# Optimization experiments

Measured on AMD Instinct MI355X. Metric: run time of the kernel, lower is better.

## Reference

```python
import jax, jax.numpy as jnp
import numpy as np
from jax import lax

MAX_DEPTH = 8
NLEAVES = 2 ** MAX_DEPTH      # 256
NNODES = 2 ** MAX_DEPTH - 1   # 255 (preorder-numbered inner nodes)
NCLASS = 10
EPS = 1e-5
BATCH = 8192


def _build_paths():
    # Reproduce the torch preorder node numbering and DFS leaf numbering.
    node_ctr = [0]
    leaf_paths = []
    def rec(depth, path):
        idx = node_ctr[0]; node_ctr[0] += 1
        if depth < MAX_DEPTH:
            rec(depth + 1, path + [(idx, 0)])   # left child: prob (1 - p)
            rec(depth + 1, path + [(idx, 1)])   # right child: prob p
        else:
            leaf_paths.append(path + [(idx, 0)])
            leaf_paths.append(path + [(idx, 1)])
    rec(1, [])
    nidx = np.array([[n for n, _ in p] for p in leaf_paths], dtype=np.int32)  # [L, D]
    dirs = np.array([[d for _, d in p] for p in leaf_paths], dtype=bool)      # [L, D]
    return nidx, dirs

NODE_IDX, DIRS = _build_paths()


def _bn(x, g, b):
    # training-mode batchnorm over all dims except channel axis 1 (biased var)
    axes = tuple(i for i in range(x.ndim) if i != 1)
    m = x.mean(axes, keepdims=True)
    v = x.var(axes, keepdims=True)
    shape = [1] * x.ndim; shape[1] = -1
    return (x - m) * lax.rsqrt(v + EPS) * g.reshape(shape) + b.reshape(shape)


def _conv(x, w, b):
    y = lax.conv_general_dilated(x, w, (1, 1), 'VALID',
                                 dimension_numbers=('NCHW', 'OIHW', 'NCHW'))
    return y + b[None, :, None, None]


def _pool2(x):
    return lax.reduce_window(x, -jnp.inf, lax.max, (1, 1, 2, 2), (1, 1, 2, 2), 'VALID')


def setup_inputs() -> dict:
    ks = jax.random.split(jax.random.key(0), 12)
    f32 = jnp.float32
    return {
        'x': jax.random.normal(ks[0], (BATCH, 1, 28, 28), f32),
        'y': jax.random.randint(ks[1], (BATCH,), 0, NCLASS),
        'conv1_w': 0.1 * jax.random.normal(ks[2], (20, 1, 5, 5), f32),
        'conv1_b': jnp.zeros((20,), f32),
        'conv2_w': 0.05 * jax.random.normal(ks[3], (50, 20, 5, 5), f32),
        'conv2_b': jnp.zeros((50,), f32),
        'g1': jnp.ones((20,), f32), 'be1': jnp.zeros((20,), f32),
        'g2': jnp.ones((50,), f32), 'be2': jnp.zeros((50,), f32),
        'fc1_w': 0.05 * jax.random.normal(ks[4], (10, 800), f32),
        'fc1_b': jnp.zeros((10,), f32),
        'g3': jnp.ones((10,), f32), 'be3': jnp.zeros((10,), f32),
        'theta_w': 0.3 * jax.random.normal(ks[5], (NNODES, 10), f32),
        'theta_b': jnp.zeros((NNODES,), f32),
        'pi': jax.random.uniform(ks[6], (NLEAVES, NCLASS), f32, 0.1, 1.0),
    }


def reference(x, y, conv1_w, conv1_b, conv2_w, conv2_b, g1, be1, g2, be2,
              fc1_w, fc1_b, g3, be3, theta_w, theta_b, pi):
    B = x.shape[0]
    # CNN backbone
    h = _pool2(jax.nn.relu(_bn(_conv(x, conv1_w, conv1_b), g1, be1)))
    h = _pool2(jax.nn.relu(_bn(_conv(h, conv2_w, conv2_b), g2, be2)))
    h = h.reshape(B, 4 * 4 * 50)
    h = jax.nn.relu(_bn(h @ fc1_w.T + fc1_b, g3, be3))        # [B, 10]
    # batched soft-tree gating: one fused GEMM for all 255 tiny Linear(10,1)
    p = jax.nn.sigmoid(h @ theta_w.T + theta_b)                # [B, NNODES]
    g = p[:, NODE_IDX]                                         # [B, L, D]
    mu = jnp.prod(jnp.where(DIRS[None], g, 1.0 - g), axis=2)   # [B, L]
    # pi is a row-stochastic distribution (uniform at torch init)
    pi_n = pi / pi.sum(1, keepdims=True)
    # stale P from __init__: uniform mu (1/L) @ pi  ->  column means of pi
    P_prev = jnp.broadcast_to(pi_n.mean(0), (B, NCLASS))       # [B, C]
    # vectorized cal_pi (soft-EM update of leaf distributions)
    Y = jax.nn.one_hot(y, NCLASS, dtype=mu.dtype)              # [B, C]
    S = mu.T @ (Y / P_prev)                                    # [L, C]
    pi_h = pi_n * S
    pi_new = pi_h / pi_h.sum(1, keepdims=True)
    # cal_P and log
    P = mu @ pi_new                                            # [B, C]
    return jnp.log(P)
```

## Files before the change

### kernel.cpp

```cpp
#include <hip/hip_runtime.h>
#include <hip/hip_bf16.h>
#include <math.h>

typedef __attribute__((ext_vector_type(8))) short short8v;
typedef __attribute__((ext_vector_type(4))) float float4v;

static const size_t F_RAWP1B = 0;
static const size_t F_C2P    = 14155776;
static const size_t F_PART1  = 20709376;
static const size_t F_PART2  = 21037056;
static const size_t F_PART3  = 21241856;
static const size_t F_BN1    = 21246976;
static const size_t F_BN2    = 21247016;
static const size_t F_SRAW   = 21247136;
static const size_t F_WB2    = 21252256;
static const size_t F_WB1    = 21271712;
static const size_t F_SPART  = 21272224;
static const size_t F_HRAW   = 0;
static const size_t F_MU     = 81920;

__device__ __forceinline__ float relu_(float v) { return v > 0.f ? v : 0.f; }

__device__ __forceinline__ unsigned int pack_bf16x2(float a, float b) {
  __hip_bfloat16 ha = __float2bfloat16(a), hb = __float2bfloat16(b);
  unsigned short ua, ub;
  __builtin_memcpy(&ua, &ha, 2); __builtin_memcpy(&ub, &hb, 2);
  return ((unsigned int)ub << 16) | ua;
}

__device__ __forceinline__ unsigned short cvt_bf16(float a) {
  __hip_bfloat16 h = __float2bfloat16(a);
  unsigned short u; __builtin_memcpy(&u, &h, 2);
  return u;
}

__device__ __forceinline__ float pick_(float a, float b, bool mx) {
  return mx ? fmaxf(a, b) : fminf(a, b);
}

__global__ __launch_bounds__(256) void k_wprep(
    const float* __restrict__ w1, const float* __restrict__ w2,
    unsigned short* __restrict__ wb1, unsigned short* __restrict__ wb2)
{
  const int gi = blockIdx.x * 256 + threadIdx.x;
  if (gi < 1024) {
    const int n = gi >> 5, k = gi & 31;
    const int kh = k / 6, kw = k - kh*6;
    float v = (n < 20 && kh < 5 && kw < 5) ? w1[n*25 + kh*5 + kw] : 0.f;
    wb1[gi] = cvt_bf16(v);
  } else {
    const int idx = gi - 1024;
    const int cc = idx >> 9;
    const int rem = idx & 511;
    const int n = rem >> 3, j = rem & 7;
    float v = 0.f;
    if (cc < 75 && n < 50) {
      const int khw = cc / 3, icg = cc - khw*3;
      const int ic = icg*8 + j;
      if (ic < 20) {
        const int kh = khw / 5, kw = khw - kh*5;
        v = w2[((n*20 + ic)*5 + kh)*5 + kw];
      }
    }
    wb2[idx] = cvt_bf16(v);
  }
}

__global__ __launch_bounds__(256) void k_conv1_mfma(
    const float* __restrict__ x, const unsigned short* __restrict__ wb1,
    const float* __restrict__ g1, unsigned int* __restrict__ rawp1b,
    float* __restrict__ part)
{
  __shared__ alignas(16) unsigned short xpk[2][1568];
  __shared__ float sred[4][32], qred[4][32];
  const int tid = threadIdx.x, blk = blockIdx.x;
  const int img0 = blk * 4;
  const int wave = tid >> 6, lane = tid & 63, lo = lane & 15, hi = lane >> 4;

  const short8v bfr0 = *(const short8v*)(wb1 + (lo*32 + hi*8));
  const short8v bfr1 = *(const short8v*)(wb1 + ((16+lo)*32 + hi*8));
  const unsigned enc = (hi==0) ? 0x0E020100u
                     : (hi==1) ? 0x1D1C100Fu
                     : (hi==2) ? 0x2C2B2A1Eu
                     :           0x003A3938u;
  const int off0 = enc & 255, off1 = (enc>>8)&255, off2 = (enc>>16)&255, off3 = enc>>24;
  const int pb   = (lo & 1) * 392;
  const int oyp  = (lo >> 1) & 1, qoff = lo >> 2;
  const int inv  = pb + (6*wave + oyp)*14;
  const bool gp0 = (g1[lo] >= 0.f);
  const bool gp1 = (lo < 4) ? (g1[16+lo] >= 0.f) : true;
  const int sr = tid >> 3, sq = tid & 7;
  const bool act = (tid < 224) && (sq < 7);
  const int su0 = sr*7 + sq;
  const int su1 = 196 + su0;

  float4 sv = make_float4(0.f, 0.f, 0.f, 0.f);
  if (act) sv = *(const float4*)(x + (size_t)img0 * 784 + sr*28 + 4*sq);
  {
    float n0 = __shfl_down(sv.x, 1);
    n0 = (sq == 6) ? 0.f : n0;
    if (act) {
      uint2* xb2 = (uint2*)&xpk[0][0];
      uint2 t0; t0.x = pack_bf16x2(sv.x, sv.y); t0.y = pack_bf16x2(sv.z, sv.w);
      uint2 t1; t1.x = pack_bf16x2(sv.y, sv.z); t1.y = pack_bf16x2(sv.w, n0);
      xb2[su0] = t0;
      xb2[su1] = t1;
    }
  }
  __syncthreads();

  float bs0[3] = {0.f, 0.f, 0.f}, bq0[3] = {0.f, 0.f, 0.f};
  float bs1[3] = {0.f, 0.f, 0.f}, bq1[3] = {0.f, 0.f, 0.f};
  int cur = 0;
  for (int ii = 0; ii < 4; ++ii) {
    if (ii < 3 && act)
      sv = *(const float4*)(x + (size_t)(img0 + ii + 1) * 784 + sr*28 + 4*sq);
    const unsigned int* xpd = (const unsigned int*)&xpk[cur][0];
    unsigned int* dst = rawp1b + (size_t)(img0 + ii) * 1728;

    #pragma unroll 1
    for (int g = 0; g < 3; ++g) {
      float4v acc[3][2];
      #pragma unroll
      for (int t3 = 0; t3 < 3; ++t3) {
        acc[t3][0] = (float4v){0.f,0.f,0.f,0.f};
        acc[t3][1] = (float4v){0.f,0.f,0.f,0.f};
      }
      #pragma unroll
      for (int t3 = 0; t3 < 3; ++t3) {
        const int base = inv + g*28 + t3*4 + qoff;
        union { unsigned int u[4]; short8v v; } cu;
        cu.u[0] = xpd[base + off0];
        cu.u[1] = xpd[base + off1];
        cu.u[2] = xpd[base + off2];
        cu.u[3] = xpd[base + off3];
        acc[t3][0] = __builtin_amdgcn_mfma_f32_16x16x32_bf16(cu.v, bfr0, acc[t3][0], 0, 0, 0);
        acc[t3][1] = __builtin_amdgcn_mfma_f32_16x16x32_bf16(cu.v, bfr1, acc[t3][1], 0, 0, 0);
      }
      #pragma unroll
      for (int t3 = 0; t3 < 3; ++t3) {
        const int T = wave*9 + g*3 + t3;
        const int q = T*4 + hi;
        const float4v v0 = acc[t3][0];
        const float4v v1 = acc[t3][1];
        #pragma unroll
        for (int r = 0; r < 4; ++r) { bs0[t3] += v0[r]; bq0[t3] += v0[r]*v0[r]; }
        #pragma unroll
        for (int r = 0; r < 4; ++r) { bs1[t3] += v1[r]; bq1[t3] += v1[r]*v1[r]; }
        const float p0 = pick_(pick_(v0[0], v0[1], gp0), pick_(v0[2], v0[3], gp0), gp0);
        const float p1 = pick_(pick_(v1[0], v1[1], gp1), pick_(v1[2], v1[3], gp1), gp1);
        const float o0 = __shfl_down(p0, 1);
        const float o1 = __shfl_down(p1, 1);
        if ((lo & 1) == 0) {
          dst[q*12 + (lo >> 1)] = pack_bf16x2(p0, o0);
          if (lo < 8)
            dst[q*12 + 8 + (lo >> 1)] = pack_bf16x2(p1, o1);
        }
      }
    }

    if (ii < 3) {
      float n0 = __shfl_down(sv.x, 1);
      n0 = (sq == 6) ? 0.f : n0;
      if (act) {
        uint2* xb2 = (uint2*)&xpk[cur ^ 1][0];
        uint2 t0; t0.x = pack_bf16x2(sv.x, sv.y); t0.y = pack_bf16x2(sv.z, sv.w);
        uint2 t1; t1.x = pack_bf16x2(sv.y, sv.z); t1.y = pack_bf16x2(sv.w, n0);
        xb2[su0] = t0;
        xb2[su1] = t1;
      }
    }
    __syncthreads();
    cur ^= 1;
  }

  float bsv0 = bs0[0] + bs0[1] + bs0[2], bqv0 = bq0[0] + bq0[1] + bq0[2];
  float bsv1 = bs1[0] + bs1[1] + bs1[2], bqv1 = bq1[0] + bq1[1] + bq1[2];
  bsv0 += __shfl_down(bsv0, 32); bqv0 += __shfl_down(bqv0, 32);
  bsv0 += __shfl_down(bsv0, 16); bqv0 += __shfl_down(bqv0, 16);
  bsv1 += __shfl_down(bsv1, 32); bqv1 += __shfl_down(bqv1, 32);
  bsv1 += __shfl_down(bsv1, 16); bqv1 += __shfl_down(bqv1, 16);
  if (hi == 0) {
    sred[wave][lo] = bsv0; sred[wave][16+lo] = bsv1;
    qred[wave][lo] = bqv0; qred[wave][16+lo] = bqv1;
  }
  __syncthreads();
  if (tid < 20) {
    float s = 0.f, q = 0.f;
    #pragma unroll
    for (int w2 = 0; w2 < 4; ++w2) { s += sred[w2][tid]; q += qred[w2][tid]; }
    part[(size_t)blk*40 + tid]      = s;
    part[(size_t)blk*40 + 20 + tid] = q;
  }
}

__global__ __launch_bounds__(256) void k_conv2_mfma(
    const unsigned int* __restrict__ rawp1b, const unsigned short* __restrict__ wb,
    const float* __restrict__ bn1, const float* __restrict__ g2,
    float* __restrict__ c2p, float* __restrict__ part)
{
  __shared__ alignas(16) unsigned int in4[6912];
  __shared__ float sred[4][64], qred[4][64];
  __shared__ alignas(16) float bn1i[48];
  __shared__ unsigned short aofft[76];
  const int tid = threadIdx.x, blk = blockIdx.x;
  if (tid < 24) {
    const float sc = (tid < 20) ? bn1[tid]      : 0.f;
    const float sh = (tid < 20) ? bn1[20 + tid] : 0.f;
    bn1i[2*tid] = sc; bn1i[2*tid + 1] = sh;
  }
  if (tid < 76) {
    const int cc2 = tid > 74 ? 74 : tid;
    const int khw = cc2 / 3, icg = cc2 - khw*3;
    const int kh = khw / 5, kw = khw - kh*5;
    aofft[tid] = (unsigned short)((kh*12 + kw)*48 + icg*16);
  }
  __syncthreads();

  const uint4* src4 = (const uint4*)(rawp1b + (size_t)blk * 6912);
  uint4* dst4 = (uint4*)in4;
  int jj = tid % 3;
  for (int k = 0; k < 7; ++k) {
    const int i = k*256 + tid;
    if (i < 1728) {
      const uint4 v = src4[i];
      unsigned int o[4];
      #pragma unroll
      for (int m = 0; m < 4; ++m) {
        const float4 ss = *(const float4*)(bn1i + jj*16 + m*4);
        const unsigned int u = (m==0) ? v.x : (m==1) ? v.y : (m==2) ? v.z : v.w;
        const float a = __uint_as_float(u << 16);
        const float b = __uint_as_float(u & 0xffff0000u);
        const float ra = relu_(fmaf(a, ss.x, ss.y));
        const float rb = relu_(fmaf(b, ss.z, ss.w));
        o[m] = pack_bf16x2(ra, rb);
      }
      uint4 ov; ov.x = o[0]; ov.y = o[1]; ov.z = o[2]; ov.w = o[3];
      dst4[i] = ov;
    }
    jj = (jj == 2) ? 0 : jj + 1;
  }
  __syncthreads();

  const int wave = tid >> 6, lane = tid & 63;
  const int lo = lane & 15, hi = lane >> 4;
  const char* ibase = (const char*)in4 + wave * 6912;

  const char* bA[4];
  #pragma unroll
  for (int a = 0; a < 4; ++a) {
    const int m = a*16 + lo;
    bA[a] = ibase + ((m >> 3) * 12 + (m & 7)) * 48;
  }
  unsigned short aoffs[19];
  #pragma unroll
  for (int s = 0; s < 19; ++s) aoffs[s] = aofft[s*4 + hi];
  const unsigned short* wbase = wb + hi*512 + lo*8;

  bool gpos[4];
  #pragma unroll
  for (int nf = 0; nf < 4; ++nf) {
    const int n = nf*16 + lo;
    gpos[nf] = (n < 50) ? (g2[n] >= 0.f) : true;
  }

  float4v acc[4][4];
  #pragma unroll
  for (int a = 0; a < 4; ++a)
    #pragma unroll
    for (int nf = 0; nf < 4; ++nf) acc[a][nf] = (float4v){0.f, 0.f, 0.f, 0.f};

  #pragma unroll
  for (int s = 0; s < 19; ++s) {
    short8v av[4], bv[4];
    #pragma unroll
    for (int am = 0; am < 4; ++am)
      av[am] = *(const short8v*)(bA[am] + aoffs[s]);
    const unsigned short* wrow = wbase + s*2048;
    #pragma unroll
    for (int nf = 0; nf < 4; ++nf)
      bv[nf] = *(const short8v*)(wrow + nf*128);
    #pragma unroll
    for (int am = 0; am < 4; ++am)
      #pragma unroll
      for (int nf = 0; nf < 4; ++nf)
        acc[am][nf] = __builtin_amdgcn_mfma_f32_16x16x32_bf16(av[am], bv[nf], acc[am][nf], 0, 0, 0);
  }

  const int img = blk*4 + wave;
  #pragma unroll
  for (int nf = 0; nf < 4; ++nf) {
    const int n = nf*16 + lo;
    float sv = 0.f, qv = 0.f;
    #pragma unroll
    for (int am = 0; am < 4; ++am) {
      float4v v = acc[am][nf];
      #pragma unroll
      for (int r = 0; r < 4; ++r) { sv += v[r]; qv += v[r]*v[r]; }
      float h0 = gpos[nf] ? fmaxf(v[0], v[1]) : fminf(v[0], v[1]);
      float h1 = gpos[nf] ? fmaxf(v[2], v[3]) : fminf(v[2], v[3]);
      const float o0 = __shfl_xor(h0, 32);
      const float o1 = __shfl_xor(h1, 32);
      h0 = gpos[nf] ? fmaxf(h0, o0) : fminf(h0, o0);
      h1 = gpos[nf] ? fmaxf(h1, o1) : fminf(h1, o1);
      if (hi < 2 && n < 50) {
        float2 o; o.x = h0; o.y = h1;
        *(float2*)(c2p + (size_t)img*800 + n*16 + am*4 + hi*2) = o;
      }
    }
    sv += __shfl_down(sv, 32); qv += __shfl_down(qv, 32);
    sv += __shfl_down(sv, 16); qv += __shfl_down(qv, 16);
    if (hi == 0) { sred[wave][nf*16 + lo] = sv; qred[wave][nf*16 + lo] = qv; }
  }
  __syncthreads();
  if (tid < 100) {
    const int ch = tid < 50 ? tid : tid - 50;
    float t = 0.f;
    if (tid < 50) {
      #pragma unroll
      for (int w2 = 0; w2 < 4; ++w2) t += sred[w2][ch];
      part[(size_t)blk*100 + ch] = t;
    } else {
      #pragma unroll
      for (int w2 = 0; w2 < 4; ++w2) t += qred[w2][ch];
      part[(size_t)blk*100 + 50 + ch] = t;
    }
  }
}

__global__ __launch_bounds__(256) void k_bn_fin(
    const float* __restrict__ part, int nblk, int nch, float N,
    const float* __restrict__ g, const float* __restrict__ b,
    float* __restrict__ out)
{
  __shared__ double rd[4][2];
  const int tid = threadIdx.x, ch = blockIdx.x;
  const int lane = tid & 63, wid = tid >> 6;
  double s = 0.0, q = 0.0;
  for (int i = tid; i < nblk; i += 256) {
    s += (double)part[(size_t)i*2*nch + ch];
    q += (double)part[(size_t)i*2*nch + nch + ch];
  }
  #pragma unroll
  for (int off = 32; off > 0; off >>= 1) { s += __shfl_down(s, off); q += __shfl_down(q, off); }
  if (lane == 0) { rd[wid][0] = s; rd[wid][1] = q; }
  __syncthreads();
  if (tid == 0) {
    double S = rd[0][0] + rd[1][0] + rd[2][0] + rd[3][0];
    double Q = rd[0][1] + rd[1][1] + rd[2][1] + rd[3][1];
    double mean = S / (double)N;
    double var  = Q / (double)N - mean * mean;
    if (var < 0.0) var = 0.0;
    float scv = (float)((double)g[ch] / sqrt(var + 1e-5));
    out[ch]       = scv;
    out[nch + ch] = b[ch] - (float)mean * scv;
  }
}

__global__ __launch_bounds__(256) void k_fc1(
    const float* __restrict__ c2p, const float* __restrict__ bn2,
    const float* __restrict__ fw, float* __restrict__ h_raw,
    float* __restrict__ part)
{
  __shared__ alignas(16) float wl[8000];
  __shared__ float s2[50], h2[50];
  __shared__ float red[4][20];
  const int tid = threadIdx.x;
  for (int i = tid; i < 2000; i += 256)
    ((float4*)wl)[i] = ((const float4*)fw)[i];
  if (tid < 50) { s2[tid] = bn2[tid]; h2[tid] = bn2[50 + tid]; }
  __syncthreads();
  const int s = tid >> 3, kc = tid & 7;
  const int sample = blockIdx.x * 32 + s;
  const float* xr = c2p + (size_t)sample * 800 + kc * 100;
  float acc[10];
  #pragma unroll
  for (int f = 0; f < 10; ++f) acc[f] = 0.f;
  #pragma unroll 5
  for (int c = 0; c < 25; ++c) {
    const int k = kc*100 + c*4;
    float4 v = *(const float4*)(xr + c*4);
    const int oc = k >> 4;
    const float sc = s2[oc], sh = h2[oc];
    v.x = relu_(v.x*sc + sh); v.y = relu_(v.y*sc + sh);
    v.z = relu_(v.z*sc + sh); v.w = relu_(v.w*sc + sh);
    #pragma unroll
    for (int f = 0; f < 10; ++f) {
      const float4 wv = *(const float4*)(wl + f*800 + k);
      acc[f] += v.x*wv.x + v.y*wv.y + v.z*wv.z + v.w*wv.w;
    }
  }
  const int lane = tid & 63, wid = tid >> 6;
  #pragma unroll
  for (int f = 0; f < 10; ++f) {
    acc[f] += __shfl_down(acc[f], 4);
    acc[f] += __shfl_down(acc[f], 2);
    acc[f] += __shfl_down(acc[f], 1);
    float a2 = (kc == 0) ? acc[f] : 0.f;
    float q2 = (kc == 0) ? acc[f]*acc[f] : 0.f;
    if (kc == 0) h_raw[(size_t)sample*10 + f] = acc[f];
    a2 += __shfl_down(a2, 32); q2 += __shfl_down(q2, 32);
    a2 += __shfl_down(a2, 16); q2 += __shfl_down(q2, 16);
    a2 += __shfl_down(a2, 8);  q2 += __shfl_down(q2, 8);
    if (lane == 0) { red[wid][f] = a2; red[wid][10+f] = q2; }
  }
  __syncthreads();
  if (tid < 20) {
    float t = 0.f;
    #pragma unroll
    for (int w2 = 0; w2 < 4; ++w2) t += red[w2][tid];
    part[(size_t)blockIdx.x*20 + tid] = t;
  }
}

__global__ __launch_bounds__(256) void k_theta_mu(
    const float* __restrict__ h_raw, const float* __restrict__ part3,
    const float* __restrict__ g3, const float* __restrict__ be3,
    const float* __restrict__ tw, const float* __restrict__ tb,
    const int* __restrict__ y, float* __restrict__ mu,
    float* __restrict__ spart)
{
  __shared__ float twt[10][256];
  __shared__ float tbl[256];
  __shared__ float hl[32][10];
  __shared__ float pl[32][256];
  __shared__ float red3[4][20];
  __shared__ float bn3s[20];
  __shared__ int   ycls[32];
  const int tid = threadIdx.x, blk = blockIdx.x;
  const int lane = tid & 63, wid = tid >> 6;

  for (int i = tid; i < 2550; i += 256) {
    const int node = i / 10, f = i - node*10;
    twt[f][node] = tw[i];
  }
  if (tid < 10) twt[tid][255] = 0.f;
  tbl[tid] = (tid < 255) ? tb[tid] : 0.f;
  if (tid < 32) ycls[tid] = y[blk*32 + tid];

  float p3[20];
  {
    const float* pr = part3 + (size_t)tid * 20;
    #pragma unroll
    for (int j = 0; j < 20; ++j) p3[j] = pr[j];
    #pragma unroll
    for (int off = 32; off > 0; off >>= 1) {
      #pragma unroll
      for (int j = 0; j < 20; ++j) p3[j] += __shfl_down(p3[j], off);
    }
    if (lane == 0) {
      #pragma unroll
      for (int j = 0; j < 20; ++j) red3[wid][j] = p3[j];
    }
  }
  __syncthreads();
  if (tid < 10) {
    double S = 0.0, Q = 0.0;
    #pragma unroll
    for (int w2 = 0; w2 < 4; ++w2) { S += red3[w2][tid]; Q += red3[w2][10+tid]; }
    double mean = S / 8192.0;
    double var  = Q / 8192.0 - mean*mean;
    if (var < 0.0) var = 0.0;
    float scv = (float)((double)g3[tid] / sqrt(var + 1e-5));
    bn3s[tid]      = scv;
    bn3s[10 + tid] = be3[tid] - (float)mean * scv;
  }
  __syncthreads();

  for (int i = tid; i < 320; i += 256) {
    const int ss = i / 10, f = i - ss*10;
    hl[ss][f] = relu_(h_raw[(size_t)blk*320 + i] * bn3s[f] + bn3s[10 + f]);
  }
  __syncthreads();

  const int node = tid;
  for (int i2 = 0; i2 < 32; ++i2) {
    float h[10];
    #pragma unroll
    for (int f = 0; f < 10; ++f) h[f] = hl[i2][f];
    float d = tbl[node];
    #pragma unroll
    for (int f = 0; f < 10; ++f) d += h[f] * twt[f][node];
    pl[i2][node] = (node < 255) ? 1.f / (1.f + __expf(-d)) : 0.f;
  }
  __syncthreads();

  float sacc[10];
  #pragma unroll
  for (int c = 0; c < 10; ++c) sacc[c] = 0.f;
  for (int i2 = 0; i2 < 32; ++i2) {
    float m = 1.f; int idx = 0;
    #pragma unroll
    for (int k = 0; k < 8; ++k) {
      const int dir = (tid >> (7 - k)) & 1;
      const float pv = pl[i2][idx];
      m *= dir ? pv : (1.f - pv);
      idx += dir ? (1 << (7 - k)) : 1;
    }
    mu[(size_t)(blk*32 + i2)*256 + tid] = m;
    const int c = ycls[i2];
    #pragma unroll
    for (int cc = 0; cc < 10; ++cc) sacc[cc] += (c == cc) ? m : 0.f;
  }
  float* dst = spart + (size_t)blk*2560 + tid*10;
  #pragma unroll
  for (int cc = 0; cc < 10; ++cc) dst[cc] = sacc[cc];
}

__global__ __launch_bounds__(256) void k_S_red(
    const float* __restrict__ spart, float* __restrict__ S)
{
  const int e = blockIdx.x * 256 + threadIdx.x;
  float s = 0.f;
  for (int k = 0; k < 256; ++k) s += spart[(size_t)k*2560 + e];
  S[e] = s;
}

__global__ __launch_bounds__(256) void k_out(
    const float* __restrict__ mu, const float* __restrict__ pi,
    const float* __restrict__ S, float* __restrict__ out)
{
  __shared__ float plt[10][260];
  __shared__ float wred[4][10];
  const int tid = threadIdx.x;
  const int lane = tid & 63, wid = tid >> 6;

  float row[10]; float rs = 0.f;
  #pragma unroll
  for (int c = 0; c < 10; ++c) { row[c] = pi[tid*10 + c]; rs += row[c]; }
  #pragma unroll
  for (int c = 0; c < 10; ++c) row[c] /= rs;
  float pp[10];
  #pragma unroll
  for (int c = 0; c < 10; ++c) pp[c] = row[c];
  #pragma unroll
  for (int off = 32; off > 0; off >>= 1) {
    #pragma unroll
    for (int c = 0; c < 10; ++c) pp[c] += __shfl_down(pp[c], off);
  }
  if (lane == 0) {
    #pragma unroll
    for (int c = 0; c < 10; ++c) wred[wid][c] = pp[c];
  }
  __syncthreads();
  float hs = 0.f; float ph[10];
  #pragma unroll
  for (int c = 0; c < 10; ++c) {
    const float Pp = (wred[0][c] + wred[1][c] + wred[2][c] + wred[3][c]) * (1.f/256.f);
    const float Sv = S[tid*10 + c] / Pp;
    ph[c] = row[c] * Sv;
    hs += ph[c];
  }
  const float ih = 1.f / hs;
  #pragma unroll
  for (int c = 0; c < 10; ++c) plt[c][tid] = ph[c] * ih;
  __syncthreads();

  const int gid = blockIdx.x * 256 + tid;
  const int b = gid / 10, c = gid % 10;
  const float4* mr4 = (const float4*)(mu + (size_t)b * 256);
  const float*  pc  = &plt[c][0];
  float a0 = 0.f, a1 = 0.f;
  #pragma unroll 4
  for (int l4 = 0; l4 < 64; ++l4) {
    const float4 m = mr4[l4];
    const float4 p = *(const float4*)(pc + 4*l4);
    a0 += m.x*p.x + m.y*p.y;
    a1 += m.z*p.z + m.w*p.w;
  }
  out[gid] = logf(a0 + a1);
}

extern "C" void kernel_launch(void* const* d_in, const int* in_sizes, int n_in,
                              void* d_out, int out_size, void* d_ws, size_t ws_size,
                              hipStream_t stream)
{
  const float* x   = (const float*)d_in[0];
  const int*   y   = (const int*)  d_in[1];
  const float* c1w = (const float*)d_in[2];
  const float* c2w = (const float*)d_in[4];
  const float* g1  = (const float*)d_in[6];
  const float* be1 = (const float*)d_in[7];
  const float* g2  = (const float*)d_in[8];
  const float* be2 = (const float*)d_in[9];
  const float* fw  = (const float*)d_in[10];
  const float* g3  = (const float*)d_in[12];
  const float* be3 = (const float*)d_in[13];
  const float* thw = (const float*)d_in[14];
  const float* thb = (const float*)d_in[15];
  const float* pi  = (const float*)d_in[16];
  float* ws  = (float*)d_ws;
  float* out = (float*)d_out;

  unsigned int*   rawp1b = (unsigned int*)(ws + F_RAWP1B);
  float*          c2p    = ws + F_C2P;
  float*          part1  = ws + F_PART1;
  float*          part2  = ws + F_PART2;
  float*          part3  = ws + F_PART3;
  float*          bn1    = ws + F_BN1;
  float*          bn2    = ws + F_BN2;
  float*          sraw   = ws + F_SRAW;
  unsigned short* wb2    = (unsigned short*)(ws + F_WB2);
  unsigned short* wb1    = (unsigned short*)(ws + F_WB1);
  float*          spart  = ws + F_SPART;
  float*          hraw   = ws + F_HRAW;
  float*          muB    = ws + F_MU;

  k_wprep<<<156, 256, 0, stream>>>(c1w, c2w, wb1, wb2);
  k_conv1_mfma<<<2048, 256, 0, stream>>>(x, wb1, g1, rawp1b, part1);
  k_bn_fin<<<20, 256, 0, stream>>>(part1, 2048, 20, 8192.f * 576.f, g1, be1, bn1);
  k_conv2_mfma<<<2048, 256, 0, stream>>>(rawp1b, wb2, bn1, g2, c2p, part2);
  k_bn_fin<<<50, 256, 0, stream>>>(part2, 2048, 50, 8192.f * 64.f, g2, be2, bn2);
  k_fc1<<<256, 256, 0, stream>>>(c2p, bn2, fw, hraw, part3);
  k_theta_mu<<<256, 256, 0, stream>>>(hraw, part3, g3, be3, thw, thb, y, muB, spart);
  k_S_red<<<10, 256, 0, stream>>>(spart, sraw);
  k_out<<<320, 256, 0, stream>>>(muB, pi, sraw, out);
}
```

Baseline: 162.6 us.

## Halve conv2 block size and transpose BN partial-sum layout for coalesced reduction

Conv2 now runs two images per 128-thread block across twice as many blocks, which halves LDS use per block and may raise occupancy. The BN partial sums from conv1 and conv2 are stored channel-major, so the finalize kernel reads them contiguously instead of with a large stride. The S reduction loop is also unrolled into four independent accumulators to expose more memory-level parallelism. Doubling the block count doubles the number of partial sums to reduce and repeats the per-block setup more often.

```diff
diff --git a/kernel.cpp b/kernel.cpp
--- a/kernel.cpp
+++ b/kernel.cpp
@@ -8,14 +8,14 @@
 static const size_t F_RAWP1B = 0;
 static const size_t F_C2P    = 14155776;
 static const size_t F_PART1  = 20709376;
-static const size_t F_PART2  = 21037056;
-static const size_t F_PART3  = 21241856;
-static const size_t F_BN1    = 21246976;
-static const size_t F_BN2    = 21247016;
-static const size_t F_SRAW   = 21247136;
-static const size_t F_WB2    = 21252256;
-static const size_t F_WB1    = 21271712;
-static const size_t F_SPART  = 21272224;
+static const size_t F_PART2  = 20791296;
+static const size_t F_PART3  = 21200896;
+static const size_t F_BN1    = 21206016;
+static const size_t F_BN2    = 21206056;
+static const size_t F_SRAW   = 21206156;
+static const size_t F_WB2    = 21208716;
+static const size_t F_WB1    = 21228172;
+static const size_t F_SPART  = 21228684;
 static const size_t F_HRAW   = 0;
 static const size_t F_MU     = 81920;
 
@@ -189,18 +189,18 @@
     float s = 0.f, q = 0.f;
     #pragma unroll
     for (int w2 = 0; w2 < 4; ++w2) { s += sred[w2][tid]; q += qred[w2][tid]; }
-    part[(size_t)blk*40 + tid]      = s;
-    part[(size_t)blk*40 + 20 + tid] = q;
-  }
-}
-
-__global__ __launch_bounds__(256) void k_conv2_mfma(
+    part[(size_t)tid*2048 + blk]        = s;
+    part[(size_t)(20 + tid)*2048 + blk] = q;
+  }
+}
+
+__global__ __launch_bounds__(128) void k_conv2_mfma(
     const unsigned int* __restrict__ rawp1b, const unsigned short* __restrict__ wb,
     const float* __restrict__ bn1, const float* __restrict__ g2,
     float* __restrict__ c2p, float* __restrict__ part)
 {
-  __shared__ alignas(16) unsigned int in4[6912];
-  __shared__ float sred[4][64], qred[4][64];
+  __shared__ alignas(16) unsigned int in4[3456];
+  __shared__ float sred[2][64], qred[2][64];
   __shared__ alignas(16) float bn1i[48];
   __shared__ unsigned short aofft[76];
   const int tid = threadIdx.x, blk = blockIdx.x;
@@ -209,20 +209,21 @@
     const float sh = (tid < 20) ? bn1[20 + tid] : 0.f;
     bn1i[2*tid] = sc; bn1i[2*tid + 1] = sh;
   }
-  if (tid < 76) {
-    const int cc2 = tid > 74 ? 74 : tid;
+  if (tid >= 32 && tid < 108) {
+    const int t = tid - 32;
+    const int cc2 = t > 74 ? 74 : t;
     const int khw = cc2 / 3, icg = cc2 - khw*3;
     const int kh = khw / 5, kw = khw - kh*5;
-    aofft[tid] = (unsigned short)((kh*12 + kw)*48 + icg*16);
-  }
-  __syncthreads();
-
-  const uint4* src4 = (const uint4*)(rawp1b + (size_t)blk * 6912);
+    aofft[t] = (unsigned short)((kh*12 + kw)*48 + icg*16);
+  }
+  __syncthreads();
+
+  const uint4* src4 = (const uint4*)(rawp1b + (size_t)blk * 3456);
   uint4* dst4 = (uint4*)in4;
   int jj = tid % 3;
   for (int k = 0; k < 7; ++k) {
-    const int i = k*256 + tid;
-    if (i < 1728) {
+    const int i = k*128 + tid;
+    if (i < 864) {
       const uint4 v = src4[i];
       unsigned int o[4];
       #pragma unroll
@@ -238,7 +239,7 @@
       uint4 ov; ov.x = o[0]; ov.y = o[1]; ov.z = o[2]; ov.w = o[3];
       dst4[i] = ov;
     }
-    jj = (jj == 2) ? 0 : jj + 1;
+    jj = (jj >= 1) ? jj - 1 : 2;
   }
   __syncthreads();
 
@@ -287,7 +288,7 @@
         acc[am][nf] = __builtin_amdgcn_mfma_f32_16x16x32_bf16(av[am], bv[nf], acc[am][nf], 0, 0, 0);
   }
 
-  const int img = blk*4 + wave;
+  const int img = blk*2 + wave;
   #pragma unroll
   for (int nf = 0; nf < 4; ++nf) {
     const int n = nf*16 + lo;
@@ -315,15 +316,10 @@
   __syncthreads();
   if (tid < 100) {
     const int ch = tid < 50 ? tid : tid - 50;
-    float t = 0.f;
     if (tid < 50) {
-      #pragma unroll
-      for (int w2 = 0; w2 < 4; ++w2) t += sred[w2][ch];
-      part[(size_t)blk*100 + ch] = t;
+      part[(size_t)ch*4096 + blk]        = sred[0][ch] + sred[1][ch];
     } else {
-      #pragma unroll
-      for (int w2 = 0; w2 < 4; ++w2) t += qred[w2][ch];
-      part[(size_t)blk*100 + 50 + ch] = t;
+      part[(size_t)(50 + ch)*4096 + blk] = qred[0][ch] + qred[1][ch];
     }
   }
 }
@@ -336,10 +332,12 @@
   __shared__ double rd[4][2];
   const int tid = threadIdx.x, ch = blockIdx.x;
   const int lane = tid & 63, wid = tid >> 6;
+  const float* ps = part + (size_t)ch * nblk;
+  const float* pq = part + (size_t)(nch + ch) * nblk;
   double s = 0.0, q = 0.0;
   for (int i = tid; i < nblk; i += 256) {
-    s += (double)part[(size_t)i*2*nch + ch];
-    q += (double)part[(size_t)i*2*nch + nch + ch];
+    s += (double)ps[i];
+    q += (double)pq[i];
   }
   #pragma unroll
   for (int off = 32; off > 0; off >>= 1) { s += __shfl_down(s, off); q += __shfl_down(q, off); }
@@ -511,9 +509,14 @@
     const float* __restrict__ spart, float* __restrict__ S)
 {
   const int e = blockIdx.x * 256 + threadIdx.x;
-  float s = 0.f;
-  for (int k = 0; k < 256; ++k) s += spart[(size_t)k*2560 + e];
-  S[e] = s;
+  float s0 = 0.f, s1 = 0.f, s2 = 0.f, s3 = 0.f;
+  for (int k = 0; k < 256; k += 4) {
+    s0 += spart[(size_t)(k+0)*2560 + e];
+    s1 += spart[(size_t)(k+1)*2560 + e];
+    s2 += spart[(size_t)(k+2)*2560 + e];
+    s3 += spart[(size_t)(k+3)*2560 + e];
+  }
+  S[e] = (s0 + s1) + (s2 + s3);
 }
 
 __global__ __launch_bounds__(256) void k_out(
@@ -609,8 +612,8 @@
   k_wprep<<<156, 256, 0, stream>>>(c1w, c2w, wb1, wb2);
   k_conv1_mfma<<<2048, 256, 0, stream>>>(x, wb1, g1, rawp1b, part1);
   k_bn_fin<<<20, 256, 0, stream>>>(part1, 2048, 20, 8192.f * 576.f, g1, be1, bn1);
-  k_conv2_mfma<<<2048, 256, 0, stream>>>(rawp1b, wb2, bn1, g2, c2p, part2);
-  k_bn_fin<<<50, 256, 0, stream>>>(part2, 2048, 50, 8192.f * 64.f, g2, be2, bn2);
+  k_conv2_mfma<<<4096, 128, 0, stream>>>(rawp1b, wb2, bn1, g2, c2p, part2);
+  k_bn_fin<<<50, 256, 0, stream>>>(part2, 4096, 50, 8192.f * 64.f, g2, be2, bn2);
   k_fc1<<<256, 256, 0, stream>>>(c2p, bn2, fw, hraw, part3);
   k_theta_mu<<<256, 256, 0, stream>>>(hraw, part3, g3, be3, thw, thb, y, muB, spart);
   k_S_red<<<10, 256, 0, stream>>>(spart, sraw);
```

Result: slower. 175.9 us (+8.2%).

## Replace BN partial-sum buffers and finalize kernels with fixed-point atomics

Applied to the files above, without the earlier changes.

Conv1 and conv2 blocks now add their per-channel sum and sum-of-squares directly into 64-bit fixed-point global accumulators with atomicAdd, instead of writing per-block partials. The two k_bn_fin launches are removed, and the consuming kernels (conv2 and fc1) compute BN scale and shift from the accumulators at block start. A memset is added to zero the accumulators. This removes two kernel launches and their serial reductions, at the cost of 2048 blocks' atomics contending on the same addresses and fixed-point quantization of the statistics.

```diff
diff --git a/kernel.cpp b/kernel.cpp
--- a/kernel.cpp
+++ b/kernel.cpp
@@ -7,17 +7,17 @@
 
 static const size_t F_RAWP1B = 0;
 static const size_t F_C2P    = 14155776;
-static const size_t F_PART1  = 20709376;
-static const size_t F_PART2  = 21037056;
 static const size_t F_PART3  = 21241856;
-static const size_t F_BN1    = 21246976;
-static const size_t F_BN2    = 21247016;
-static const size_t F_SRAW   = 21247136;
-static const size_t F_WB2    = 21252256;
-static const size_t F_WB1    = 21271712;
-static const size_t F_SPART  = 21272224;
+static const size_t F_ACC    = 21246976;
+static const size_t F_SRAW   = 21247256;
+static const size_t F_WB2    = 21249816;
+static const size_t F_WB1    = 21269272;
+static const size_t F_SPART  = 21269784;
 static const size_t F_HRAW   = 0;
 static const size_t F_MU     = 81920;
+
+#define FXSCALE 16777216.f
+#define FXINV   (1.0/16777216.0)
 
 __device__ __forceinline__ float relu_(float v) { return v > 0.f ? v : 0.f; }
 
@@ -36,6 +36,10 @@
 
 __device__ __forceinline__ float pick_(float a, float b, bool mx) {
   return mx ? fmaxf(a, b) : fminf(a, b);
+}
+
+__device__ __forceinline__ void atom_fx(unsigned long long* p, float v) {
+  atomicAdd(p, (unsigned long long)(long long)llrintf(v * FXSCALE));
 }
 
 __global__ __launch_bounds__(256) void k_wprep(
@@ -69,7 +73,7 @@
 __global__ __launch_bounds__(256) void k_conv1_mfma(
     const float* __restrict__ x, const unsigned short* __restrict__ wb1,
     const float* __restrict__ g1, unsigned int* __restrict__ rawp1b,
-    float* __restrict__ part)
+    unsigned long long* __restrict__ acc1)
 {
   __shared__ alignas(16) unsigned short xpk[2][1568];
   __shared__ float sred[4][32], qred[4][32];
@@ -189,15 +193,17 @@
     float s = 0.f, q = 0.f;
     #pragma unroll
     for (int w2 = 0; w2 < 4; ++w2) { s += sred[w2][tid]; q += qred[w2][tid]; }
-    part[(size_t)blk*40 + tid]      = s;
-    part[(size_t)blk*40 + 20 + tid] = q;
+    atom_fx(&acc1[tid], s);
+    atom_fx(&acc1[20 + tid], q);
   }
 }
 
 __global__ __launch_bounds__(256) void k_conv2_mfma(
     const unsigned int* __restrict__ rawp1b, const unsigned short* __restrict__ wb,
-    const float* __restrict__ bn1, const float* __restrict__ g2,
-    float* __restrict__ c2p, float* __restrict__ part)
+    const unsigned long long* __restrict__ acc1,
+    const float* __restrict__ g1, const float* __restrict__ be1,
+    const float* __restrict__ g2, float* __restrict__ c2p,
+    unsigned long long* __restrict__ acc2)
 {
   __shared__ alignas(16) unsigned int in4[6912];
   __shared__ float sred[4][64], qred[4][64];
@@ -205,8 +211,16 @@
   __shared__ unsigned short aofft[76];
   const int tid = threadIdx.x, blk = blockIdx.x;
   if (tid < 24) {
-    const float sc = (tid < 20) ? bn1[tid]      : 0.f;
-    const float sh = (tid < 20) ? bn1[20 + tid] : 0.f;
+    float sc = 0.f, sh = 0.f;
+    if (tid < 20) {
+      const double S = (double)(long long)acc1[tid]      * FXINV;
+      const double Q = (double)(long long)acc1[20 + tid] * FXINV;
+      const double mean = S / 4718592.0;
+      double var = Q / 4718592.0 - mean*mean;
+      if (var < 0.0) var = 0.0;
+      sc = (float)((double)g1[tid] / sqrt(var + 1e-5));
+      sh = be1[tid] - (float)mean * sc;
+    }
     bn1i[2*tid] = sc; bn1i[2*tid + 1] = sh;
   }
   if (tid < 76) {
@@ -319,46 +333,17 @@
     if (tid < 50) {
       #pragma unroll
       for (int w2 = 0; w2 < 4; ++w2) t += sred[w2][ch];
-      part[(size_t)blk*100 + ch] = t;
     } else {
       #pragma unroll
       for (int w2 = 0; w2 < 4; ++w2) t += qred[w2][ch];
-      part[(size_t)blk*100 + 50 + ch] = t;
-    }
-  }
-}
-
-__global__ __launch_bounds__(256) void k_bn_fin(
-    const float* __restrict__ part, int nblk, int nch, float N,
-    const float* __restrict__ g, const float* __restrict__ b,
-    float* __restrict__ out)
-{
-  __shared__ double rd[4][2];
-  const int tid = threadIdx.x, ch = blockIdx.x;
-  const int lane = tid & 63, wid = tid >> 6;
-  double s = 0.0, q = 0.0;
-  for (int i = tid; i < nblk; i += 256) {
-    s += (double)part[(size_t)i*2*nch + ch];
-    q += (double)part[(size_t)i*2*nch + nch + ch];
-  }
-  #pragma unroll
-  for (int off = 32; off > 0; off >>= 1) { s += __shfl_down(s, off); q += __shfl_down(q, off); }
-  if (lane == 0) { rd[wid][0] = s; rd[wid][1] = q; }
-  __syncthreads();
-  if (tid == 0) {
-    double S = rd[0][0] + rd[1][0] + rd[2][0] + rd[3][0];
-    double Q = rd[0][1] + rd[1][1] + rd[2][1] + rd[3][1];
-    double mean = S / (double)N;
-    double var  = Q / (double)N - mean * mean;
-    if (var < 0.0) var = 0.0;
-    float scv = (float)((double)g[ch] / sqrt(var + 1e-5));
-    out[ch]       = scv;
-    out[nch + ch] = b[ch] - (float)mean * scv;
+    }
+    atom_fx(&acc2[tid], t);
   }
 }
 
 __global__ __launch_bounds__(256) void k_fc1(
-    const float* __restrict__ c2p, const float* __restrict__ bn2,
+    const float* __restrict__ c2p, const unsigned long long* __restrict__ acc2,
+    const float* __restrict__ g2, const float* __restrict__ be2,
     const float* __restrict__ fw, float* __restrict__ h_raw,
     float* __restrict__ part)
 {
@@ -368,7 +353,16 @@
   const int tid = threadIdx.x;
   for (int i = tid; i < 2000; i += 256)
     ((float4*)wl)[i] = ((const float4*)fw)[i];
-  if (tid < 50) { s2[tid] = bn2[tid]; h2[tid] = bn2[50 + tid]; }
+  if (tid < 50) {
+    const double S = (double)(long long)acc2[tid]      * FXINV;
+    const double Q = (double)(long long)acc2[50 + tid] * FXINV;
+    const double mean = S / 524288.0;
+    double var = Q / 524288.0 - mean*mean;
+    if (var < 0.0) var = 0.0;
+    const float sc = (float)((double)g2[tid] / sqrt(var + 1e-5));
+    s2[tid] = sc;
+    h2[tid] = be2[tid] - (float)mean * sc;
+  }
   __syncthreads();
   const int s = tid >> 3, kc = tid & 7;
   const int sample = blockIdx.x * 32 + s;
@@ -592,26 +586,24 @@
   float* ws  = (float*)d_ws;
   float* out = (float*)d_out;
 
-  unsigned int*   rawp1b = (unsigned int*)(ws + F_RAWP1B);
-  float*          c2p    = ws + F_C2P;
-  float*          part1  = ws + F_PART1;
-  float*          part2  = ws + F_PART2;
-  float*          part3  = ws + F_PART3;
-  float*          bn1    = ws + F_BN1;
-  float*          bn2    = ws + F_BN2;
-  float*          sraw   = ws + F_SRAW;
-  unsigned short* wb2    = (unsigned short*)(ws + F_WB2);
-  unsigned short* wb1    = (unsigned short*)(ws + F_WB1);
-  float*          spart  = ws + F_SPART;
-  float*          hraw   = ws + F_HRAW;
-  float*          muB    = ws + F_MU;
+  unsigned int*       rawp1b = (unsigned int*)(ws + F_RAWP1B);
+  float*              c2p    = ws + F_C2P;
+  float*              part3  = ws + F_PART3;
+  unsigned long long* acc1   = (unsigned long long*)(ws + F_ACC);
+  unsigned long long* acc2   = acc1 + 40;
+  float*              sraw   = ws + F_SRAW;
+  unsigned short*     wb2    = (unsigned short*)(ws + F_WB2);
+  unsigned short*     wb1    = (unsigned short*)(ws + F_WB1);
+  float*              spart  = ws + F_SPART;
+  float*              hraw   = ws + F_HRAW;
+  float*              muB    = ws + F_MU;
+
+  hipMemsetAsync(acc1, 0, 140 * sizeof(unsigned long long), stream);
 
   k_wprep<<<156, 256, 0, stream>>>(c1w, c2w, wb1, wb2);
-  k_conv1_mfma<<<2048, 256, 0, stream>>>(x, wb1, g1, rawp1b, part1);
-  k_bn_fin<<<20, 256, 0, stream>>>(part1, 2048, 20, 8192.f * 576.f, g1, be1, bn1);
-  k_conv2_mfma<<<2048, 256, 0, stream>>>(rawp1b, wb2, bn1, g2, c2p, part2);
-  k_bn_fin<<<50, 256, 0, stream>>>(part2, 2048, 50, 8192.f * 64.f, g2, be2, bn2);
-  k_fc1<<<256, 256, 0, stream>>>(c2p, bn2, fw, hraw, part3);
+  k_conv1_mfma<<<2048, 256, 0, stream>>>(x, wb1, g1, rawp1b, acc1);
+  k_conv2_mfma<<<2048, 256, 0, stream>>>(rawp1b, wb2, acc1, g1, be1, g2, c2p, acc2);
+  k_fc1<<<256, 256, 0, stream>>>(c2p, acc2, g2, be2, fw, hraw, part3);
   k_theta_mu<<<256, 256, 0, stream>>>(hraw, part3, g3, be3, thw, thb, y, muB, spart);
   k_S_red<<<10, 256, 0, stream>>>(spart, sraw);
   k_out<<<320, 256, 0, stream>>>(muB, pi, sraw, out);
```

After: 253.6 us. +56.0%, slower.
